# Kernel optimization log

Measured on AMD Instinct MI355X. Metric: run time of the kernel, lower is better.

The kernel has to match this reference:

```python
import jax, jax.numpy as jnp
import numpy as np

DIM = 256
QK_DIM = 256
NUM_HEADS = 8
N_WIN = 7
TOPK = 4
SCALE = QK_DIM ** (-0.5)


def setup_inputs() -> dict:
    key = jax.random.key(0)
    k1, k2, k3 = jax.random.split(key, 3)
    N, D, H, W, C = 2, 8, 56, 56, DIM
    x = jax.random.normal(k1, (N, D, H, W, C), dtype=jnp.float32)
    # QKVLinear: Linear(dim, qk_dim + qk_dim + dim)
    Wqkv = jax.random.normal(k2, (C, 2 * QK_DIM + DIM), dtype=jnp.float32) * 0.02
    bqkv = jnp.zeros((2 * QK_DIM + DIM,), dtype=jnp.float32)
    Wo = jax.random.normal(k3, (DIM, DIM), dtype=jnp.float32) * 0.02
    bo = jnp.zeros((DIM,), dtype=jnp.float32)
    return {"x": x, "Wqkv": Wqkv, "bqkv": bqkv, "Wo": Wo, "bo": bo}


def reference(x, Wqkv, bqkv, Wo, bo):
    N, D, H, W, C = x.shape
    j = i = N_WIN
    h, w = H // j, W // i
    p2, w2 = j * i, h * w
    n = N * D
    m = NUM_HEADS
    ch = QK_DIM // m   # qk head dim
    cv = DIM // m      # v head dim

    # n t (j h) (i w) c -> n t (j i) h w c
    xw = x.reshape(N, D, j, h, i, w, C).transpose(0, 1, 2, 4, 3, 5, 6)
    xw = xw.reshape(N, D, p2, h, w, C)

    # QKVLinear then split into q / kv
    qkv = xw @ Wqkv + bqkv                       # (N,D,p2,h,w,2qk+dim)
    q = qkv[..., :QK_DIM]                        # (N,D,p2,h,w,qk)
    kv = qkv[..., QK_DIM:]                       # (N,D,p2,h,w,qk+dim)

    # inter-frame shift: frame t uses kv of frame t+1; last frame keeps its own
    kv = jnp.concatenate([kv[:, 1:], kv[:, -1:]], axis=1)

    q = q.reshape(n, p2, h, w, QK_DIM)
    kv = kv.reshape(n, p2, h, w, QK_DIM + DIM)
    q_pix = q.reshape(n, p2, w2, QK_DIM)
    kv_pix = kv.reshape(n, p2, w2, QK_DIM + DIM)  # identity kv_down

    # window-level routing (diff_routing=False -> detached)
    q_win = jax.lax.stop_gradient(q.mean(axis=(2, 3)))                  # (n,p2,qk)
    k_win = jax.lax.stop_gradient(kv[..., :QK_DIM].mean(axis=(2, 3)))   # (n,p2,qk)
    attn_logit = jnp.einsum('npc,nqc->npq', q_win * SCALE, k_win)       # (n,p2,p2)
    topk_logit, r_idx = jax.lax.top_k(attn_logit, TOPK)                 # (n,p2,topk)
    r_weight = jax.nn.softmax(topk_logit, axis=-1)  # computed, unused (mul_weight='none')

    # gather kv of routed windows: (n,p2,topk,w2,qk+dim)
    kv_sel = jax.vmap(lambda kvp, idx: kvp[idx])(kv_pix, r_idx)

    k_sel = kv_sel[..., :QK_DIM].reshape(n, p2, TOPK * w2, m, ch)
    v_sel = kv_sel[..., QK_DIM:].reshape(n, p2, TOPK * w2, m, cv)
    qh = q_pix.reshape(n, p2, w2, m, ch)

    attn = jnp.einsum('npqmc,npkmc->npmqk', qh * SCALE, k_sel)  # (n,p2,m,w2,topk*w2)
    attn = jax.nn.softmax(attn, axis=-1)
    out = jnp.einsum('npmqk,npkmc->npqmc', attn, v_sel).reshape(n, p2, w2, C)

    # (n j i) (h w) c -> N D (j h) (i w) c
    out = out.reshape(N, D, j, i, h, w, C).transpose(0, 1, 2, 4, 3, 5, 6)
    out = out.reshape(N, D, H, W, C)
    out = out @ Wo + bo
    return out
```

## Files before the change

kernel.cpp:

```cpp
#include <hip/hip_runtime.h>
#include <hip/hip_bf16.h>
#include <math.h>

#define QSC 0.09016844f

typedef __attribute__((ext_vector_type(8))) short bf16x8;
typedef __attribute__((ext_vector_type(4))) float f32x4;

__device__ __forceinline__ ushort f2bf(float f) {
    unsigned u = __float_as_uint(f);
    return (ushort)((u + 0x7FFFu + ((u >> 16) & 1u)) >> 16);
}

__device__ __forceinline__ unsigned pk2bf(float a, float b) {
    __hip_bfloat162 h = __float22bfloat162_rn(make_float2(a, b));
    return *(unsigned*)&h;
}

__device__ __forceinline__ void gl_lds16(const ushort* g, ushort* l) {
    __builtin_amdgcn_global_load_lds(
        (const __attribute__((address_space(1))) unsigned int*)g,
        (__attribute__((address_space(3))) unsigned int*)l, 16, 0, 0);
}

__device__ __forceinline__ int token_to_xrow(int t) {
    int nd  = t / 3136;
    int r   = t % 3136;
    int p   = r >> 6;
    int pix = r & 63;
    int j = p / 7, i = p % 7;
    int hh = pix >> 3, ww = pix & 7;
    return nd * 3136 + (j * 8 + hh) * 56 + (i * 8 + ww);
}

__global__ __launch_bounds__(256) void k_cast_x(const float* __restrict__ x,
                                                ushort* __restrict__ xg) {
    int gid = blockIdx.x * 256 + threadIdx.x;
    int t = gid >> 6, c = (gid & 63) * 4;
    float4 v = *(const float4*)&x[(size_t)token_to_xrow(t) * 256 + c];
    ushort4 o;
    o.x = f2bf(v.x); o.y = f2bf(v.y); o.z = f2bf(v.z); o.w = f2bf(v.w);
    *(ushort4*)&xg[(size_t)t * 256 + c] = o;
}

__global__ __launch_bounds__(256) void k_cast_w(const float* __restrict__ Wqkv,
                                                const float* __restrict__ Wo,
                                                ushort* __restrict__ Wqkvt,
                                                ushort* __restrict__ Wot) {
    int b = blockIdx.x, tid = threadIdx.x;
    if (b < 768) Wqkvt[b * 256 + tid] = f2bf(Wqkv[(size_t)tid * 768 + b]);
    else { int n = b - 768; Wot[n * 256 + tid] = f2bf(Wo[(size_t)tid * 256 + n]); }
}

__global__ __launch_bounds__(256) void k_xmean(const float* __restrict__ x,
                                               float* __restrict__ xmean) {
    int b = blockIdx.x;
    int nd = b / 49, p = b % 49;
    int j = p / 7, i = p % 7;
    const float* xb = x + ((size_t)nd * 3136 + (j * 8) * 56 + i * 8) * 256 + threadIdx.x;
    float s = 0.f;
#pragma unroll
    for (int hh = 0; hh < 8; ++hh)
#pragma unroll
        for (int ww = 0; ww < 8; ++ww) s += xb[(size_t)(hh * 56 + ww) * 256];
    xmean[(size_t)b * 256 + threadIdx.x] = s * (1.f / 64.f);
}

__global__ __launch_bounds__(256) void k_winproj(const float* __restrict__ xmean,
                                                 const float* __restrict__ Wqkv,
                                                 const float* __restrict__ bqkv,
                                                 float* __restrict__ qwin,
                                                 float* __restrict__ kwin) {
    __shared__ float As[16 * 68];
    __shared__ float Bs[16 * 64];
    const int tid = threadIdx.x;
    const int m0 = blockIdx.y * 64;
    const int n0 = blockIdx.x * 64;

    const int ar = tid >> 2;
    const int ak = (tid & 3) * 4;
    const int arow = (m0 + ar < 784) ? (m0 + ar) : 783;
    const float* aptr = xmean + (size_t)arow * 256 + ak;

    const int bk = tid >> 4;
    const int bn = (tid & 15) * 4;
    const float* bptr = Wqkv + (size_t)bk * 768 + n0 + bn;

    const int ty = tid >> 4, tx = tid & 15;
    float acc[4][4] = {};

    for (int kt = 0; kt < 256; kt += 16) {
        float4 av = *(const float4*)(aptr + kt);
        float4 bv = *(const float4*)(bptr + (size_t)kt * 768);
        __syncthreads();
        As[(ak + 0) * 68 + ar] = av.x;
        As[(ak + 1) * 68 + ar] = av.y;
        As[(ak + 2) * 68 + ar] = av.z;
        As[(ak + 3) * 68 + ar] = av.w;
        *(float4*)&Bs[bk * 64 + bn] = bv;
        __syncthreads();
#pragma unroll
        for (int kk = 0; kk < 16; ++kk) {
            float4 a4 = *(const float4*)&As[kk * 68 + ty * 4];
            float4 b4 = *(const float4*)&Bs[kk * 64 + tx * 4];
            float a[4] = {a4.x, a4.y, a4.z, a4.w};
            float b[4] = {b4.x, b4.y, b4.z, b4.w};
#pragma unroll
            for (int ii = 0; ii < 4; ++ii)
#pragma unroll
                for (int jj = 0; jj < 4; ++jj) acc[ii][jj] += a[ii] * b[jj];
        }
    }
#pragma unroll
    for (int ii = 0; ii < 4; ++ii) {
        int t = m0 + ty * 4 + ii;
        if (t >= 784) continue;
#pragma unroll
        for (int jj = 0; jj < 4; ++jj) {
            int col = n0 + tx * 4 + jj;
            float v = acc[ii][jj] + bqkv[col];
            if (col < 256) qwin[(size_t)t * 256 + col] = v;
            else           kwin[(size_t)t * 256 + (col - 256)] = v;
        }
    }
}

__global__ __launch_bounds__(64) void k_route(const float* __restrict__ qwin,
                                              const float* __restrict__ kwin,
                                              int* __restrict__ ridx) {
    const int b = blockIdx.x;
    const int nd = b / 49;
    const int ndkv = ((nd & 7) == 7) ? nd : nd + 1;
    const int t = threadIdx.x;
    __shared__ float qs[256];
    for (int i = t; i < 256; i += 64) qs[i] = qwin[b * 256 + i];
    __syncthreads();
    float logit = -INFINITY;
    if (t < 49) {
        const float* kr = kwin + ((size_t)ndkv * 49 + t) * 256;
        float s = 0.f;
        for (int c = 0; c < 256; ++c) s += qs[c] * kr[c];
        logit = s;
    }
    for (int sel = 0; sel < 4; ++sel) {
        float v = logit;
        int ix = t;
        for (int off = 32; off > 0; off >>= 1) {
            float ov = __shfl_xor(v, off);
            int   oi = __shfl_xor(ix, off);
            if (ov > v || (ov == v && oi < ix)) { v = ov; ix = oi; }
        }
        if (t == 0) ridx[b * 4 + sel] = ix;
        if (t == ix) logit = -INFINITY;
    }
}

__global__ __launch_bounds__(256) void k_gemm_qkv(const ushort* __restrict__ A,
                                                  const ushort* __restrict__ Bt,
                                                  const float* __restrict__ bqkv,
                                                  ushort* __restrict__ q,
                                                  ushort* __restrict__ kv) {
    __shared__ ushort As[128 * 32];
    __shared__ ushort Bs[128 * 32];
    const int tid = threadIdx.x;
    const int wv = tid >> 6, ln = tid & 63;
    const int lane15 = ln & 15, quad = ln >> 4;
    const int m0 = blockIdx.y * 128, n0 = blockIdx.x * 128;
    const int row0 = tid >> 2, ck = tid & 3;

    const ushort* gA[2]; const ushort* gB[2];
    ushort* lA[2]; ushort* lB[2];
#pragma unroll
    for (int p = 0; p < 2; ++p) {
        gA[p] = A  + (size_t)(m0 + p * 64 + row0) * 256 + ck * 8;
        gB[p] = Bt + (size_t)(n0 + p * 64 + row0) * 256 + ck * 8;
        lA[p] = &As[(p * 256 + tid) * 8];
        lB[p] = &Bs[(p * 256 + tid) * 8];
    }

    f32x4 acc[4][4];
#pragma unroll
    for (int i = 0; i < 4; ++i)
#pragma unroll
        for (int j = 0; j < 4; ++j) acc[i][j] = (f32x4){0.f, 0.f, 0.f, 0.f};

    const int mb = (wv >> 1) * 64, nb = (wv & 1) * 64;

    for (int kt = 0; kt < 8; ++kt) {
        __syncthreads();
#pragma unroll
        for (int p = 0; p < 2; ++p) {
            gl_lds16(gA[p] + kt * 32, lA[p]);
            gl_lds16(gB[p] + kt * 32, lB[p]);
        }
        __syncthreads();
        bf16x8 aF[4], bF[4];
#pragma unroll
        for (int mt = 0; mt < 4; ++mt)
            aF[mt] = *(const bf16x8*)&As[(mb + mt * 16 + lane15) * 32 + quad * 8];
#pragma unroll
        for (int nt = 0; nt < 4; ++nt)
            bF[nt] = *(const bf16x8*)&Bs[(nb + nt * 16 + lane15) * 32 + quad * 8];
#pragma unroll
        for (int mt = 0; mt < 4; ++mt)
#pragma unroll
            for (int nt = 0; nt < 4; ++nt)
                acc[mt][nt] = __builtin_amdgcn_mfma_f32_16x16x32_bf16(aF[mt], bF[nt], acc[mt][nt], 0, 0, 0);
    }

#pragma unroll
    for (int mt = 0; mt < 4; ++mt) {
#pragma unroll
        for (int nt = 0; nt < 4; ++nt) {
            int col = n0 + nb + nt * 16 + lane15;
            float bias = bqkv[col];
#pragma unroll
            for (int r = 0; r < 4; ++r) {
                int t = m0 + mb + mt * 16 + quad * 4 + r;
                float v = acc[mt][nt][r] + bias;
                if (col < 256) q[(size_t)t * 256 + col] = f2bf(v * QSC);
                else           kv[(size_t)t * 512 + (col - 256)] = f2bf(v);
            }
        }
    }
}

__global__ __launch_bounds__(256) void k_gemm_o(const ushort* __restrict__ A,
                                                const ushort* __restrict__ Bt,
                                                const float* __restrict__ bo,
                                                float* __restrict__ out) {
    __shared__ ushort As[128 * 32];
    __shared__ ushort Bs[128 * 32];
    const int tid = threadIdx.x;
    const int wv = tid >> 6, ln = tid & 63;
    const int lane15 = ln & 15, quad = ln >> 4;
    const int m0 = blockIdx.y * 128, n0 = blockIdx.x * 128;
    const int row0 = tid >> 2, ck = tid & 3;

    const ushort* gA[2]; const ushort* gB[2];
    ushort* lA[2]; ushort* lB[2];
#pragma unroll
    for (int p = 0; p < 2; ++p) {
        gA[p] = A  + (size_t)(m0 + p * 64 + row0) * 256 + ck * 8;
        gB[p] = Bt + (size_t)(n0 + p * 64 + row0) * 256 + ck * 8;
        lA[p] = &As[(p * 256 + tid) * 8];
        lB[p] = &Bs[(p * 256 + tid) * 8];
    }

    f32x4 acc[4][4];
#pragma unroll
    for (int i = 0; i < 4; ++i)
#pragma unroll
        for (int j = 0; j < 4; ++j) acc[i][j] = (f32x4){0.f, 0.f, 0.f, 0.f};

    const int mb = (wv >> 1) * 64, nb = (wv & 1) * 64;

    for (int kt = 0; kt < 8; ++kt) {
        __syncthreads();
#pragma unroll
        for (int p = 0; p < 2; ++p) {
            gl_lds16(gA[p] + kt * 32, lA[p]);
            gl_lds16(gB[p] + kt * 32, lB[p]);
        }
        __syncthreads();
        bf16x8 aF[4], bF[4];
#pragma unroll
        for (int mt = 0; mt < 4; ++mt)
            aF[mt] = *(const bf16x8*)&As[(mb + mt * 16 + lane15) * 32 + quad * 8];
#pragma unroll
        for (int nt = 0; nt < 4; ++nt)
            bF[nt] = *(const bf16x8*)&Bs[(nb + nt * 16 + lane15) * 32 + quad * 8];
#pragma unroll
        for (int mt = 0; mt < 4; ++mt)
#pragma unroll
            for (int nt = 0; nt < 4; ++nt)
                acc[mt][nt] = __builtin_amdgcn_mfma_f32_16x16x32_bf16(aF[mt], bF[nt], acc[mt][nt], 0, 0, 0);
    }

#pragma unroll
    for (int mt = 0; mt < 4; ++mt) {
#pragma unroll
        for (int nt = 0; nt < 4; ++nt) {
            int col = n0 + nb + nt * 16 + lane15;
            float bias = bo[col];
#pragma unroll
            for (int r = 0; r < 4; ++r) {
                int t = m0 + mb + mt * 16 + quad * 4 + r;
                int xr = token_to_xrow(t);
                out[(size_t)xr * 256 + col] = acc[mt][nt][r] + bias;
            }
        }
    }
}

__global__ __launch_bounds__(256, 3) void k_attn(ushort* qbuf,
                                                 const ushort* __restrict__ kvbuf,
                                                 const int* __restrict__ ridx) {
    const int h = blockIdx.x, p = blockIdx.y, nd = blockIdx.z;
    const int ndkv = ((nd & 7) == 7) ? nd : nd + 1;
    const int tid = threadIdx.x;
    const int wv = tid >> 6, ln = tid & 63;
    const int lane15 = ln & 15, quad = ln >> 4;

    __shared__ ushort Ks[256 * 40];
    __shared__ ushort Vt[32 * 264];
    __shared__ ushort Ps[64 * 72];

    const int rb = (nd * 49 + p) * 4;
    int wid[4];
#pragma unroll
    for (int i = 0; i < 4; ++i) wid[i] = ridx[rb + i];

    const size_t kvband = (size_t)ndkv * 49;

    {
        int pix = tid >> 2, ck = tid & 3;
#pragma unroll
        for (int i = 0; i < 4; ++i) {
            size_t trow = (kvband + wid[i]) * 64 + pix;
            bf16x8 v = *(const bf16x8*)(kvbuf + trow * 512 + h * 32 + ck * 8);
            *(bf16x8*)&Ks[(i * 64 + pix) * 40 + ck * 8] = v;
        }
    }
    {
        int key_l = (tid & 31) * 2;
        int ch0 = (tid >> 5) * 4;
#pragma unroll
        for (int i = 0; i < 4; ++i) {
            size_t trow = (kvband + wid[i]) * 64;
            const ushort* g0 = kvbuf + (trow + key_l) * 512 + 256 + h * 32 + ch0;
            const ushort* g1 = g0 + 512;
            ushort4 a = *(const ushort4*)g0;
            ushort4 b = *(const ushort4*)g1;
            int kg = i * 64 + key_l;
            *(unsigned*)&Vt[(ch0 + 0) * 264 + kg] = (unsigned)a.x | ((unsigned)b.x << 16);
            *(unsigned*)&Vt[(ch0 + 1) * 264 + kg] = (unsigned)a.y | ((unsigned)b.y << 16);
            *(unsigned*)&Vt[(ch0 + 2) * 264 + kg] = (unsigned)a.z | ((unsigned)b.z << 16);
            *(unsigned*)&Vt[(ch0 + 3) * 264 + kg] = (unsigned)a.w | ((unsigned)b.w << 16);
        }
    }

    const size_t qrow0 = (size_t)(nd * 49 + p) * 64;
    bf16x8 bQ = *(const bf16x8*)(qbuf + (qrow0 + wv * 16 + lane15) * 256 + h * 32 + quad * 8);

    __syncthreads();

    f32x4 st[16];
#pragma unroll
    for (int t = 0; t < 16; ++t) {
        bf16x8 aK = *(const bf16x8*)&Ks[(t * 16 + lane15) * 40 + quad * 8];
        st[t] = __builtin_amdgcn_mfma_f32_16x16x32_bf16(aK, bQ, (f32x4){0.f, 0.f, 0.f, 0.f}, 0, 0, 0);
    }

    float sum = 0.f;
#pragma unroll
    for (int t = 0; t < 16; ++t)
#pragma unroll
        for (int r = 0; r < 4; ++r) {
            float e = __builtin_amdgcn_exp2f(st[t][r]);
            st[t][r] = e;
            sum += e;
        }
    sum += __shfl_xor(sum, 16);
    sum += __shfl_xor(sum, 32);
    const float inv = 1.f / sum;

    f32x4 oacc[2] = {{0.f, 0.f, 0.f, 0.f}, {0.f, 0.f, 0.f, 0.f}};
    const int prow = (wv * 16 + lane15) * 72;
#pragma unroll
    for (int cc = 0; cc < 4; ++cc) {
#pragma unroll
        for (int tt = 0; tt < 4; ++tt) {
            int t = cc * 4 + tt;
            uint2 pk;
            pk.x = pk2bf(st[t][0], st[t][1]);
            pk.y = pk2bf(st[t][2], st[t][3]);
            *(uint2*)&Ps[prow + tt * 16 + quad * 4] = pk;
        }
#pragma unroll
        for (int kt = 0; kt < 2; ++kt) {
            bf16x8 aP = *(const bf16x8*)&Ps[prow + kt * 32 + quad * 8];
#pragma unroll
            for (int nt = 0; nt < 2; ++nt) {
                bf16x8 bV = *(const bf16x8*)&Vt[(nt * 16 + lane15) * 264 + cc * 64 + kt * 32 + quad * 8];
                oacc[nt] = __builtin_amdgcn_mfma_f32_16x16x32_bf16(aP, bV, oacc[nt], 0, 0, 0);
            }
        }
    }

#pragma unroll
    for (int nt = 0; nt < 2; ++nt)
#pragma unroll
        for (int r = 0; r < 4; ++r) {
            int row = wv * 16 + quad * 4 + r;
            qbuf[(qrow0 + row) * 256 + h * 32 + nt * 16 + lane15] = f2bf(oacc[nt][r] * inv);
        }
}

extern "C" void kernel_launch(void* const* d_in, const int* in_sizes, int n_in,
                              void* d_out, int out_size, void* d_ws, size_t ws_size,
                              hipStream_t stream) {
    const float* x    = (const float*)d_in[0];
    const float* Wqkv = (const float*)d_in[1];
    const float* bqkv = (const float*)d_in[2];
    const float* Wo   = (const float*)d_in[3];
    const float* bo   = (const float*)d_in[4];
    float* out = (float*)d_out;

    char* ws = (char*)d_ws;
    ushort* xg    = (ushort*)ws;                    ws += (size_t)50176 * 256 * 2;
    ushort* q     = (ushort*)ws;                    ws += (size_t)50176 * 256 * 2;
    ushort* kv    = (ushort*)ws;                    ws += (size_t)50176 * 512 * 2;
    ushort* Wqkvt = (ushort*)ws;                    ws += (size_t)768 * 256 * 2;
    ushort* Wot   = (ushort*)ws;                    ws += (size_t)256 * 256 * 2;
    float*  xmean = (float*)ws;                     ws += (size_t)784 * 256 * 4;
    float*  qwin  = (float*)ws;                     ws += (size_t)784 * 256 * 4;
    float*  kwin  = (float*)ws;                     ws += (size_t)784 * 256 * 4;
    int*    ridx  = (int*)ws;

    k_cast_w  <<<1024, 256, 0, stream>>>(Wqkv, Wo, Wqkvt, Wot);
    k_cast_x  <<<12544, 256, 0, stream>>>(x, xg);
    k_xmean   <<<784, 256, 0, stream>>>(x, xmean);
    k_winproj <<<dim3(8, 13), 256, 0, stream>>>(xmean, Wqkv, bqkv, qwin, kwin);
    k_route   <<<784, 64, 0, stream>>>(qwin, kwin, ridx);
    k_gemm_qkv<<<dim3(6, 392), 256, 0, stream>>>(xg, Wqkvt, bqkv, q, kv);
    k_attn    <<<dim3(8, 49, 16), 256, 0, stream>>>(q, kv, ridx);
    k_gemm_o  <<<dim3(2, 392), 256, 0, stream>>>(q, Wot, bo, out);
}
```

Baseline: 257.6 us.

## Fuse x cast with window mean, and attention with output projection

Merges the permuted bf16 cast of x into the window-mean kernel so x is read once. Fuses the attention kernel with the output projection: each block now loops over all 8 heads for one window, keeps the attention output in LDS, and multiplies it by Wo read straight from global memory, which removes the q-buffer round trip and one launch. It also adds an XOR swizzle to the QKV GEMM's LDS tiles to reduce bank conflicts. The cost is a grid of only 784 blocks, each doing serial per-head work with more LDS, so occupancy and parallelism drop.

```diff
diff --git a/kernel.cpp b/kernel.cpp
--- a/kernel.cpp
+++ b/kernel.cpp
@@ -23,25 +23,7 @@
         (__attribute__((address_space(3))) unsigned int*)l, 16, 0, 0);
 }
 
-__device__ __forceinline__ int token_to_xrow(int t) {
-    int nd  = t / 3136;
-    int r   = t % 3136;
-    int p   = r >> 6;
-    int pix = r & 63;
-    int j = p / 7, i = p % 7;
-    int hh = pix >> 3, ww = pix & 7;
-    return nd * 3136 + (j * 8 + hh) * 56 + (i * 8 + ww);
-}
-
-__global__ __launch_bounds__(256) void k_cast_x(const float* __restrict__ x,
-                                                ushort* __restrict__ xg) {
-    int gid = blockIdx.x * 256 + threadIdx.x;
-    int t = gid >> 6, c = (gid & 63) * 4;
-    float4 v = *(const float4*)&x[(size_t)token_to_xrow(t) * 256 + c];
-    ushort4 o;
-    o.x = f2bf(v.x); o.y = f2bf(v.y); o.z = f2bf(v.z); o.w = f2bf(v.w);
-    *(ushort4*)&xg[(size_t)t * 256 + c] = o;
-}
+__device__ __forceinline__ int swz(int row) { return (row ^ (row >> 2)) & 3; }
 
 __global__ __launch_bounds__(256) void k_cast_w(const float* __restrict__ Wqkv,
                                                 const float* __restrict__ Wo,
@@ -52,17 +34,23 @@
     else { int n = b - 768; Wot[n * 256 + tid] = f2bf(Wo[(size_t)tid * 256 + n]); }
 }
 
-__global__ __launch_bounds__(256) void k_xmean(const float* __restrict__ x,
-                                               float* __restrict__ xmean) {
+__global__ __launch_bounds__(256) void k_prep(const float* __restrict__ x,
+                                              ushort* __restrict__ xg,
+                                              float* __restrict__ xmean) {
     int b = blockIdx.x;
     int nd = b / 49, p = b % 49;
     int j = p / 7, i = p % 7;
     const float* xb = x + ((size_t)nd * 3136 + (j * 8) * 56 + i * 8) * 256 + threadIdx.x;
+    ushort* xo = xg + (size_t)b * 64 * 256 + threadIdx.x;
     float s = 0.f;
-#pragma unroll
+#pragma unroll 2
     for (int hh = 0; hh < 8; ++hh)
 #pragma unroll
-        for (int ww = 0; ww < 8; ++ww) s += xb[(size_t)(hh * 56 + ww) * 256];
+        for (int ww = 0; ww < 8; ++ww) {
+            float v = xb[(size_t)(hh * 56 + ww) * 256];
+            s += v;
+            xo[(size_t)(hh * 8 + ww) * 256] = f2bf(v);
+        }
     xmean[(size_t)b * 256 + threadIdx.x] = s * (1.f / 64.f);
 }
 
@@ -166,14 +154,16 @@
     const int wv = tid >> 6, ln = tid & 63;
     const int lane15 = ln & 15, quad = ln >> 4;
     const int m0 = blockIdx.y * 128, n0 = blockIdx.x * 128;
-    const int row0 = tid >> 2, ck = tid & 3;
+    const int row0 = tid >> 2, ck0 = tid & 3;
 
     const ushort* gA[2]; const ushort* gB[2];
     ushort* lA[2]; ushort* lB[2];
 #pragma unroll
     for (int p = 0; p < 2; ++p) {
-        gA[p] = A  + (size_t)(m0 + p * 64 + row0) * 256 + ck * 8;
-        gB[p] = Bt + (size_t)(n0 + p * 64 + row0) * 256 + ck * 8;
+        int r = p * 64 + row0;
+        int cks = ck0 ^ swz(r);
+        gA[p] = A  + (size_t)(m0 + r) * 256 + cks * 8;
+        gB[p] = Bt + (size_t)(n0 + r) * 256 + cks * 8;
         lA[p] = &As[(p * 256 + tid) * 8];
         lB[p] = &Bs[(p * 256 + tid) * 8];
     }
@@ -196,11 +186,15 @@
         __syncthreads();
         bf16x8 aF[4], bF[4];
 #pragma unroll
-        for (int mt = 0; mt < 4; ++mt)
-            aF[mt] = *(const bf16x8*)&As[(mb + mt * 16 + lane15) * 32 + quad * 8];
-#pragma unroll
-        for (int nt = 0; nt < 4; ++nt)
-            bF[nt] = *(const bf16x8*)&Bs[(nb + nt * 16 + lane15) * 32 + quad * 8];
+        for (int mt = 0; mt < 4; ++mt) {
+            int r = mb + mt * 16 + lane15;
+            aF[mt] = *(const bf16x8*)&As[r * 32 + (quad ^ swz(r)) * 8];
+        }
+#pragma unroll
+        for (int nt = 0; nt < 4; ++nt) {
+            int r = nb + nt * 16 + lane15;
+            bF[nt] = *(const bf16x8*)&Bs[r * 32 + (quad ^ swz(r)) * 8];
+        }
 #pragma unroll
         for (int mt = 0; mt < 4; ++mt)
 #pragma unroll
@@ -225,78 +219,13 @@
     }
 }
 
-__global__ __launch_bounds__(256) void k_gemm_o(const ushort* __restrict__ A,
-                                                const ushort* __restrict__ Bt,
+__global__ __launch_bounds__(256) void k_attn_o(const ushort* __restrict__ qbuf,
+                                                const ushort* __restrict__ kvbuf,
+                                                const ushort* __restrict__ Wot,
+                                                const int* __restrict__ ridx,
                                                 const float* __restrict__ bo,
                                                 float* __restrict__ out) {
-    __shared__ ushort As[128 * 32];
-    __shared__ ushort Bs[128 * 32];
-    const int tid = threadIdx.x;
-    const int wv = tid >> 6, ln = tid & 63;
-    const int lane15 = ln & 15, quad = ln >> 4;
-    const int m0 = blockIdx.y * 128, n0 = blockIdx.x * 128;
-    const int row0 = tid >> 2, ck = tid & 3;
-
-    const ushort* gA[2]; const ushort* gB[2];
-    ushort* lA[2]; ushort* lB[2];
-#pragma unroll
-    for (int p = 0; p < 2; ++p) {
-        gA[p] = A  + (size_t)(m0 + p * 64 + row0) * 256 + ck * 8;
-        gB[p] = Bt + (size_t)(n0 + p * 64 + row0) * 256 + ck * 8;
-        lA[p] = &As[(p * 256 + tid) * 8];
-        lB[p] = &Bs[(p * 256 + tid) * 8];
-    }
-
-    f32x4 acc[4][4];
-#pragma unroll
-    for (int i = 0; i < 4; ++i)
-#pragma unroll
-        for (int j = 0; j < 4; ++j) acc[i][j] = (f32x4){0.f, 0.f, 0.f, 0.f};
-
-    const int mb = (wv >> 1) * 64, nb = (wv & 1) * 64;
-
-    for (int kt = 0; kt < 8; ++kt) {
-        __syncthreads();
-#pragma unroll
-        for (int p = 0; p < 2; ++p) {
-            gl_lds16(gA[p] + kt * 32, lA[p]);
-            gl_lds16(gB[p] + kt * 32, lB[p]);
-        }
-        __syncthreads();
-        bf16x8 aF[4], bF[4];
-#pragma unroll
-        for (int mt = 0; mt < 4; ++mt)
-            aF[mt] = *(const bf16x8*)&As[(mb + mt * 16 + lane15) * 32 + quad * 8];
-#pragma unroll
-        for (int nt = 0; nt < 4; ++nt)
-            bF[nt] = *(const bf16x8*)&Bs[(nb + nt * 16 + lane15) * 32 + quad * 8];
-#pragma unroll
-        for (int mt = 0; mt < 4; ++mt)
-#pragma unroll
-            for (int nt = 0; nt < 4; ++nt)
-                acc[mt][nt] = __builtin_amdgcn_mfma_f32_16x16x32_bf16(aF[mt], bF[nt], acc[mt][nt], 0, 0, 0);
-    }
-
-#pragma unroll
-    for (int mt = 0; mt < 4; ++mt) {
-#pragma unroll
-        for (int nt = 0; nt < 4; ++nt) {
-            int col = n0 + nb + nt * 16 + lane15;
-            float bias = bo[col];
-#pragma unroll
-            for (int r = 0; r < 4; ++r) {
-                int t = m0 + mb + mt * 16 + quad * 4 + r;
-                int xr = token_to_xrow(t);
-                out[(size_t)xr * 256 + col] = acc[mt][nt][r] + bias;
-            }
-        }
-    }
-}
-
-__global__ __launch_bounds__(256, 3) void k_attn(ushort* qbuf,
-                                                 const ushort* __restrict__ kvbuf,
-                                                 const int* __restrict__ ridx) {
-    const int h = blockIdx.x, p = blockIdx.y, nd = blockIdx.z;
+    const int p = blockIdx.x, nd = blockIdx.y;
     const int ndkv = ((nd & 7) == 7) ? nd : nd + 1;
     const int tid = threadIdx.x;
     const int wv = tid >> 6, ln = tid & 63;
@@ -305,6 +234,7 @@
     __shared__ ushort Ks[256 * 40];
     __shared__ ushort Vt[32 * 264];
     __shared__ ushort Ps[64 * 72];
+    __shared__ ushort Obuf[64 * 264];
 
     const int rb = (nd * 49 + p) * 4;
     int wid[4];
@@ -312,19 +242,22 @@
     for (int i = 0; i < 4; ++i) wid[i] = ridx[rb + i];
 
     const size_t kvband = (size_t)ndkv * 49;
-
-    {
-        int pix = tid >> 2, ck = tid & 3;
+    const size_t qrow0 = (size_t)(nd * 49 + p) * 64;
+
+    const int pix = tid >> 2, ck = tid & 3;
+    const int key_l = (tid & 31) * 2, ch0 = (tid >> 5) * 4;
+    const int prow = (wv * 16 + lane15) * 72;
+
+#pragma unroll 1
+    for (int h = 0; h < 8; ++h) {
+        __syncthreads();
+
 #pragma unroll
         for (int i = 0; i < 4; ++i) {
             size_t trow = (kvband + wid[i]) * 64 + pix;
             bf16x8 v = *(const bf16x8*)(kvbuf + trow * 512 + h * 32 + ck * 8);
             *(bf16x8*)&Ks[(i * 64 + pix) * 40 + ck * 8] = v;
         }
-    }
-    {
-        int key_l = (tid & 31) * 2;
-        int ch0 = (tid >> 5) * 4;
 #pragma unroll
         for (int i = 0; i < 4; ++i) {
             size_t trow = (kvband + wid[i]) * 64;
@@ -338,63 +271,89 @@
             *(unsigned*)&Vt[(ch0 + 2) * 264 + kg] = (unsigned)a.z | ((unsigned)b.z << 16);
             *(unsigned*)&Vt[(ch0 + 3) * 264 + kg] = (unsigned)a.w | ((unsigned)b.w << 16);
         }
-    }
-
-    const size_t qrow0 = (size_t)(nd * 49 + p) * 64;
-    bf16x8 bQ = *(const bf16x8*)(qbuf + (qrow0 + wv * 16 + lane15) * 256 + h * 32 + quad * 8);
-
+
+        bf16x8 bQ = *(const bf16x8*)(qbuf + (qrow0 + wv * 16 + lane15) * 256 + h * 32 + quad * 8);
+
+        __syncthreads();
+
+        f32x4 st[16];
+#pragma unroll
+        for (int t = 0; t < 16; ++t) {
+            bf16x8 aK = *(const bf16x8*)&Ks[(t * 16 + lane15) * 40 + quad * 8];
+            st[t] = __builtin_amdgcn_mfma_f32_16x16x32_bf16(aK, bQ, (f32x4){0.f, 0.f, 0.f, 0.f}, 0, 0, 0);
+        }
+
+        float sum = 0.f;
+#pragma unroll
+        for (int t = 0; t < 16; ++t)
+#pragma unroll
+            for (int r = 0; r < 4; ++r) {
+                float e = __builtin_amdgcn_exp2f(st[t][r]);
+                st[t][r] = e;
+                sum += e;
+            }
+        sum += __shfl_xor(sum, 16);
+        sum += __shfl_xor(sum, 32);
+        const float inv = 1.f / sum;
+
+        f32x4 oacc[2] = {{0.f, 0.f, 0.f, 0.f}, {0.f, 0.f, 0.f, 0.f}};
+#pragma unroll
+        for (int cc = 0; cc < 4; ++cc) {
+#pragma unroll
+            for (int tt = 0; tt < 4; ++tt) {
+                int t = cc * 4 + tt;
+                uint2 pk;
+                pk.x = pk2bf(st[t][0], st[t][1]);
+                pk.y = pk2bf(st[t][2], st[t][3]);
+                *(uint2*)&Ps[prow + tt * 16 + quad * 4] = pk;
+            }
+#pragma unroll
+            for (int kt = 0; kt < 2; ++kt) {
+                bf16x8 aP = *(const bf16x8*)&Ps[prow + kt * 32 + quad * 8];
+#pragma unroll
+                for (int nt = 0; nt < 2; ++nt) {
+                    bf16x8 bV = *(const bf16x8*)&Vt[(nt * 16 + lane15) * 264 + cc * 64 + kt * 32 + quad * 8];
+                    oacc[nt] = __builtin_amdgcn_mfma_f32_16x16x32_bf16(aP, bV, oacc[nt], 0, 0, 0);
+                }
+            }
+        }
+
+#pragma unroll
+        for (int nt = 0; nt < 2; ++nt)
+#pragma unroll
+            for (int r = 0; r < 4; ++r)
+                Obuf[(wv * 16 + quad * 4 + r) * 264 + h * 32 + nt * 16 + lane15] =
+                    f2bf(oacc[nt][r] * inv);
+    }
     __syncthreads();
 
-    f32x4 st[16];
-#pragma unroll
-    for (int t = 0; t < 16; ++t) {
-        bf16x8 aK = *(const bf16x8*)&Ks[(t * 16 + lane15) * 40 + quad * 8];
-        st[t] = __builtin_amdgcn_mfma_f32_16x16x32_bf16(aK, bQ, (f32x4){0.f, 0.f, 0.f, 0.f}, 0, 0, 0);
-    }
-
-    float sum = 0.f;
-#pragma unroll
-    for (int t = 0; t < 16; ++t)
-#pragma unroll
-        for (int r = 0; r < 4; ++r) {
-            float e = __builtin_amdgcn_exp2f(st[t][r]);
-            st[t][r] = e;
-            sum += e;
-        }
-    sum += __shfl_xor(sum, 16);
-    sum += __shfl_xor(sum, 32);
-    const float inv = 1.f / sum;
-
-    f32x4 oacc[2] = {{0.f, 0.f, 0.f, 0.f}, {0.f, 0.f, 0.f, 0.f}};
-    const int prow = (wv * 16 + lane15) * 72;
-#pragma unroll
-    for (int cc = 0; cc < 4; ++cc) {
-#pragma unroll
-        for (int tt = 0; tt < 4; ++tt) {
-            int t = cc * 4 + tt;
-            uint2 pk;
-            pk.x = pk2bf(st[t][0], st[t][1]);
-            pk.y = pk2bf(st[t][2], st[t][3]);
-            *(uint2*)&Ps[prow + tt * 16 + quad * 4] = pk;
-        }
-#pragma unroll
-        for (int kt = 0; kt < 2; ++kt) {
-            bf16x8 aP = *(const bf16x8*)&Ps[prow + kt * 32 + quad * 8];
-#pragma unroll
-            for (int nt = 0; nt < 2; ++nt) {
-                bf16x8 bV = *(const bf16x8*)&Vt[(nt * 16 + lane15) * 264 + cc * 64 + kt * 32 + quad * 8];
-                oacc[nt] = __builtin_amdgcn_mfma_f32_16x16x32_bf16(aP, bV, oacc[nt], 0, 0, 0);
-            }
-        }
-    }
-
-#pragma unroll
-    for (int nt = 0; nt < 2; ++nt)
+    f32x4 acc[16];
+#pragma unroll
+    for (int nt = 0; nt < 16; ++nt) acc[nt] = (f32x4){0.f, 0.f, 0.f, 0.f};
+
+#pragma unroll 1
+    for (int kt = 0; kt < 8; ++kt) {
+        bf16x8 aO = *(const bf16x8*)&Obuf[(wv * 16 + lane15) * 264 + kt * 32 + quad * 8];
+#pragma unroll
+        for (int nt = 0; nt < 16; ++nt) {
+            bf16x8 bW = *(const bf16x8*)(Wot + (size_t)(nt * 16 + lane15) * 256 + kt * 32 + quad * 8);
+            acc[nt] = __builtin_amdgcn_mfma_f32_16x16x32_bf16(aO, bW, acc[nt], 0, 0, 0);
+        }
+    }
+
+    const int j = p / 7, i = p % 7;
+#pragma unroll
+    for (int nt = 0; nt < 16; ++nt) {
+        int col = nt * 16 + lane15;
+        float bias = bo[col];
 #pragma unroll
         for (int r = 0; r < 4; ++r) {
             int row = wv * 16 + quad * 4 + r;
-            qbuf[(qrow0 + row) * 256 + h * 32 + nt * 16 + lane15] = f2bf(oacc[nt][r] * inv);
-        }
+            int hh = row >> 3, ww = row & 7;
+            int xr = nd * 3136 + (j * 8 + hh) * 56 + (i * 8 + ww);
+            out[(size_t)xr * 256 + col] = acc[nt][r] + bias;
+        }
+    }
 }
 
 extern "C" void kernel_launch(void* const* d_in, const int* in_sizes, int n_in,
@@ -419,11 +378,9 @@
     int*    ridx  = (int*)ws;
 
     k_cast_w  <<<1024, 256, 0, stream>>>(Wqkv, Wo, Wqkvt, Wot);
-    k_cast_x  <<<12544, 256, 0, stream>>>(x, xg);
-    k_xmean   <<<784, 256, 0, stream>>>(x, xmean);
+    k_prep    <<<784, 256, 0, stream>>>(x, xg, xmean);
     k_winproj <<<dim3(8, 13), 256, 0, stream>>>(xmean, Wqkv, bqkv, qwin, kwin);
     k_route   <<<784, 64, 0, stream>>>(qwin, kwin, ridx);
     k_gemm_qkv<<<dim3(6, 392), 256, 0, stream>>>(xg, Wqkvt, bqkv, q, kv);
-    k_attn    <<<dim3(8, 49, 16), 256, 0, stream>>>(q, kv, ridx);
-    k_gemm_o  <<<dim3(2, 392), 256, 0, stream>>>(q, Wot, bo, out);
-}
+    k_attn_o  <<<dim3(49, 16), 256, 0, stream>>>(q, kv, Wot, ridx, bo, out);
+}
```

Measured after the change: 319.1 us. +23.9%, slower.

## Fuse x cast, window mean and weight cast; XOR-swizzle GEMM LDS tiles

Applied to the files above, without the earlier changes.

Merges the three prep kernels into one k_prep launch. Each window block now reads x once, writing both the bf16 gathered copy and the window mean, which removes a second full read of x and two launches. Both GEMMs now place each 16-byte chunk in LDS at an XOR-swizzled column so the MFMA fragment reads avoid bank conflicts. The fused prep writes are per-thread 2-byte scalar stores rather than vector stores, and only 784 blocks do the x work, which may lower memory throughput.

```diff
diff --git a/kernel.cpp b/kernel.cpp
--- a/kernel.cpp
+++ b/kernel.cpp
@@ -22,6 +22,8 @@
         (const __attribute__((address_space(1))) unsigned int*)g,
         (__attribute__((address_space(3))) unsigned int*)l, 16, 0, 0);
 }
+
+__device__ __forceinline__ int swz(int row) { return (row ^ (row >> 2)) & 3; }
 
 __device__ __forceinline__ int token_to_xrow(int t) {
     int nd  = t / 3136;
@@ -33,37 +35,35 @@
     return nd * 3136 + (j * 8 + hh) * 56 + (i * 8 + ww);
 }
 
-__global__ __launch_bounds__(256) void k_cast_x(const float* __restrict__ x,
-                                                ushort* __restrict__ xg) {
-    int gid = blockIdx.x * 256 + threadIdx.x;
-    int t = gid >> 6, c = (gid & 63) * 4;
-    float4 v = *(const float4*)&x[(size_t)token_to_xrow(t) * 256 + c];
-    ushort4 o;
-    o.x = f2bf(v.x); o.y = f2bf(v.y); o.z = f2bf(v.z); o.w = f2bf(v.w);
-    *(ushort4*)&xg[(size_t)t * 256 + c] = o;
-}
-
-__global__ __launch_bounds__(256) void k_cast_w(const float* __restrict__ Wqkv,
-                                                const float* __restrict__ Wo,
-                                                ushort* __restrict__ Wqkvt,
-                                                ushort* __restrict__ Wot) {
-    int b = blockIdx.x, tid = threadIdx.x;
-    if (b < 768) Wqkvt[b * 256 + tid] = f2bf(Wqkv[(size_t)tid * 768 + b]);
-    else { int n = b - 768; Wot[n * 256 + tid] = f2bf(Wo[(size_t)tid * 256 + n]); }
-}
-
-__global__ __launch_bounds__(256) void k_xmean(const float* __restrict__ x,
-                                               float* __restrict__ xmean) {
+__global__ __launch_bounds__(256) void k_prep(const float* __restrict__ x,
+                                              const float* __restrict__ Wqkv,
+                                              const float* __restrict__ Wo,
+                                              ushort* __restrict__ xg,
+                                              float* __restrict__ xmean,
+                                              ushort* __restrict__ Wqkvt,
+                                              ushort* __restrict__ Wot) {
     int b = blockIdx.x;
+    int tid = threadIdx.x;
+    if (b >= 784) {
+        int bb = b - 784;
+        if (bb < 768) Wqkvt[bb * 256 + tid] = f2bf(Wqkv[(size_t)tid * 768 + bb]);
+        else { int n = bb - 768; Wot[n * 256 + tid] = f2bf(Wo[(size_t)tid * 256 + n]); }
+        return;
+    }
     int nd = b / 49, p = b % 49;
     int j = p / 7, i = p % 7;
-    const float* xb = x + ((size_t)nd * 3136 + (j * 8) * 56 + i * 8) * 256 + threadIdx.x;
+    const float* xb = x + ((size_t)nd * 3136 + (j * 8) * 56 + i * 8) * 256 + tid;
+    ushort* xo = xg + (size_t)b * 64 * 256 + tid;
     float s = 0.f;
-#pragma unroll
+#pragma unroll 2
     for (int hh = 0; hh < 8; ++hh)
 #pragma unroll
-        for (int ww = 0; ww < 8; ++ww) s += xb[(size_t)(hh * 56 + ww) * 256];
-    xmean[(size_t)b * 256 + threadIdx.x] = s * (1.f / 64.f);
+        for (int ww = 0; ww < 8; ++ww) {
+            float v = xb[(size_t)(hh * 56 + ww) * 256];
+            s += v;
+            xo[(size_t)(hh * 8 + ww) * 256] = f2bf(v);
+        }
+    xmean[(size_t)b * 256 + tid] = s * (1.f / 64.f);
 }
 
 __global__ __launch_bounds__(256) void k_winproj(const float* __restrict__ xmean,
@@ -166,14 +166,16 @@
     const int wv = tid >> 6, ln = tid & 63;
     const int lane15 = ln & 15, quad = ln >> 4;
     const int m0 = blockIdx.y * 128, n0 = blockIdx.x * 128;
-    const int row0 = tid >> 2, ck = tid & 3;
+    const int row0 = tid >> 2, ck0 = tid & 3;
 
     const ushort* gA[2]; const ushort* gB[2];
     ushort* lA[2]; ushort* lB[2];
 #pragma unroll
     for (int p = 0; p < 2; ++p) {
-        gA[p] = A  + (size_t)(m0 + p * 64 + row0) * 256 + ck * 8;
-        gB[p] = Bt + (size_t)(n0 + p * 64 + row0) * 256 + ck * 8;
+        int r = p * 64 + row0;
+        int cks = ck0 ^ swz(r);
+        gA[p] = A  + (size_t)(m0 + r) * 256 + cks * 8;
+        gB[p] = Bt + (size_t)(n0 + r) * 256 + cks * 8;
         lA[p] = &As[(p * 256 + tid) * 8];
         lB[p] = &Bs[(p * 256 + tid) * 8];
     }
@@ -196,11 +198,15 @@
         __syncthreads();
         bf16x8 aF[4], bF[4];
 #pragma unroll
-        for (int mt = 0; mt < 4; ++mt)
-            aF[mt] = *(const bf16x8*)&As[(mb + mt * 16 + lane15) * 32 + quad * 8];
-#pragma unroll
-        for (int nt = 0; nt < 4; ++nt)
-            bF[nt] = *(const bf16x8*)&Bs[(nb + nt * 16 + lane15) * 32 + quad * 8];
+        for (int mt = 0; mt < 4; ++mt) {
+            int r = mb + mt * 16 + lane15;
+            aF[mt] = *(const bf16x8*)&As[r * 32 + (quad ^ swz(r)) * 8];
+        }
+#pragma unroll
+        for (int nt = 0; nt < 4; ++nt) {
+            int r = nb + nt * 16 + lane15;
+            bF[nt] = *(const bf16x8*)&Bs[r * 32 + (quad ^ swz(r)) * 8];
+        }
 #pragma unroll
         for (int mt = 0; mt < 4; ++mt)
 #pragma unroll
@@ -235,14 +241,16 @@
     const int wv = tid >> 6, ln = tid & 63;
     const int lane15 = ln & 15, quad = ln >> 4;
     const int m0 = blockIdx.y * 128, n0 = blockIdx.x * 128;
-    const int row0 = tid >> 2, ck = tid & 3;
+    const int row0 = tid >> 2, ck0 = tid & 3;
 
     const ushort* gA[2]; const ushort* gB[2];
     ushort* lA[2]; ushort* lB[2];
 #pragma unroll
     for (int p = 0; p < 2; ++p) {
-        gA[p] = A  + (size_t)(m0 + p * 64 + row0) * 256 + ck * 8;
-        gB[p] = Bt + (size_t)(n0 + p * 64 + row0) * 256 + ck * 8;
+        int r = p * 64 + row0;
+        int cks = ck0 ^ swz(r);
+        gA[p] = A  + (size_t)(m0 + r) * 256 + cks * 8;
+        gB[p] = Bt + (size_t)(n0 + r) * 256 + cks * 8;
         lA[p] = &As[(p * 256 + tid) * 8];
         lB[p] = &Bs[(p * 256 + tid) * 8];
     }
@@ -265,11 +273,15 @@
         __syncthreads();
         bf16x8 aF[4], bF[4];
 #pragma unroll
-        for (int mt = 0; mt < 4; ++mt)
-            aF[mt] = *(const bf16x8*)&As[(mb + mt * 16 + lane15) * 32 + quad * 8];
-#pragma unroll
-        for (int nt = 0; nt < 4; ++nt)
-            bF[nt] = *(const bf16x8*)&Bs[(nb + nt * 16 + lane15) * 32 + quad * 8];
+        for (int mt = 0; mt < 4; ++mt) {
+            int r = mb + mt * 16 + lane15;
+            aF[mt] = *(const bf16x8*)&As[r * 32 + (quad ^ swz(r)) * 8];
+        }
+#pragma unroll
+        for (int nt = 0; nt < 4; ++nt) {
+            int r = nb + nt * 16 + lane15;
+            bF[nt] = *(const bf16x8*)&Bs[r * 32 + (quad ^ swz(r)) * 8];
+        }
 #pragma unroll
         for (int mt = 0; mt < 4; ++mt)
 #pragma unroll
@@ -418,9 +430,7 @@
     float*  kwin  = (float*)ws;                     ws += (size_t)784 * 256 * 4;
     int*    ridx  = (int*)ws;
 
-    k_cast_w  <<<1024, 256, 0, stream>>>(Wqkv, Wo, Wqkvt, Wot);
-    k_cast_x  <<<12544, 256, 0, stream>>>(x, xg);
-    k_xmean   <<<784, 256, 0, stream>>>(x, xmean);
+    k_prep    <<<1808, 256, 0, stream>>>(x, Wqkv, Wo, xg, xmean, Wqkvt, Wot);
     k_winproj <<<dim3(8, 13), 256, 0, stream>>>(xmean, Wqkv, bqkv, qwin, kwin);
     k_route   <<<784, 64, 0, stream>>>(qwin, kwin, ridx);
     k_gemm_qkv<<<dim3(6, 392), 256, 0, stream>>>(xg, Wqkvt, bqkv, q, kv);
```

After: 253.4 us. No clear change (-1.6%).
